# Kernel optimization log

Hardware: AMD Instinct MI355X
Metric: run time of the kernel (lower is better)

## Reference

```python
import jax, jax.numpy as jnp
import numpy as np
from jax import lax

B, N, F_IN, T = 1024, 22, 32, 32
K = 3
CHEV = 64     # nb_chev_filter
TIMEF = 64    # nb_time_filter
LN_EPS = 1e-5


def setup_inputs() -> dict:
    key = jax.random.key(0)
    ks = jax.random.split(key, 19)
    rn = lambda k, shape, s=0.1: (jax.random.normal(k, shape, jnp.float32) * s)
    return {
        "x": rn(ks[0], (B, N, F_IN, T), 1.0),
        # Temporal_Attention_layer params
        "U1": rn(ks[1], (N,)),
        "U2": rn(ks[2], (F_IN, N)),
        "U3": rn(ks[3], (F_IN,)),
        "be": rn(ks[4], (1, T, T)),
        "Ve": rn(ks[5], (T, T)),
        # Spatial_Attention_layer params
        "W1": rn(ks[6], (T,)),
        "W2": rn(ks[7], (F_IN, T)),
        "W3": rn(ks[8], (F_IN,)),
        "bs": rn(ks[9], (1, N, N)),
        "Vs": rn(ks[10], (N, N)),
        # cheb_conv_withSAt params
        "Theta": rn(ks[11], (K, F_IN, CHEV)),
        "node_emb": rn(ks[12], (N, N), 1.0),
        # time conv (1x3, pad (0,1)) and residual conv (1x1)
        "tconv_w": rn(ks[13], (TIMEF, CHEV, 1, 3)),
        "tconv_b": rn(ks[14], (TIMEF,)),
        "rconv_w": rn(ks[15], (TIMEF, F_IN, 1, 1)),
        "rconv_b": rn(ks[16], (TIMEF,)),
        # LayerNorm over nb_time_filter
        "ln_g": jnp.ones((TIMEF,), jnp.float32),
        "ln_b": jnp.zeros((TIMEF,), jnp.float32),
    }


def reference(x, U1, U2, U3, be, Ve, W1, W2, W3, bs, Vs, Theta, node_emb,
              tconv_w, tconv_b, rconv_w, rconv_b, ln_g, ln_b):
    Bx, Nx, Fx, Tx = x.shape

    # ---- Temporal attention: E_normalized [B, T, T] ----
    # lhs = ((x.permute(0,3,2,1) @ U1) @ U2)  -> [B, T, N]
    lhs_t = jnp.einsum('bnft,n->btf', x, U1) @ U2          # [B,T,N]
    rhs_t = jnp.einsum('f,bnft->bnt', U3, x)               # [B,N,T]
    prod_t = jnp.einsum('btn,bns->bts', lhs_t, rhs_t)      # [B,T,T]
    E = jnp.einsum('ts,bsu->btu', Ve, jax.nn.sigmoid(prod_t + be))
    E_norm = jax.nn.softmax(E, axis=1)                     # softmax over dim=1

    # x_TAt = reshape(x, [B, N*F, T]) @ E_norm  -> [B, N, F, T]
    x_TAt = (x.reshape(Bx, Nx * Fx, Tx) @ E_norm).reshape(Bx, Nx, Fx, Tx)

    # ---- Spatial attention on x_TAt: S_normalized [B, N, N] ----
    lhs_s = jnp.einsum('bnft,t->bnf', x_TAt, W1) @ W2      # [B,N,T]
    rhs_s = jnp.einsum('f,bnft->bnt', W3, x_TAt)           # [B,N,T]
    prod_s = jnp.einsum('bnt,bmt->bnm', lhs_s, rhs_s)      # [B,N,N]
    S = jnp.einsum('nm,bml->bnl', Vs, jax.nn.sigmoid(prod_s + bs))
    S_norm = jax.nn.softmax(S, axis=1)                     # softmax over dim=1

    # ---- Chebyshev graph conv with adaptive supports (vectorized over T) ----
    supports = jax.nn.softmax(jax.nn.relu(node_emb @ node_emb.T), axis=1)
    support_set = [jnp.eye(Nx, dtype=x.dtype), supports]
    for _ in range(2, K):
        support_set.append(2.0 * supports @ support_set[-1] - support_set[-2])

    out = jnp.zeros((Bx, Nx, CHEV, Tx), x.dtype)
    for k in range(K):
        A_k = support_set[k][None, :, :] * S_norm          # [B,N,N]
        # rhs[b,m,f,t] = sum_n A_k[b,n,m] * x[b,n,f,t]  (A_k^T @ graph_signal)
        rhs = jnp.einsum('bnm,bnft->bmft', A_k, x)
        out = out + jnp.einsum('bmft,fo->bmot', rhs, Theta[k])
    spatial_gcn = jax.nn.relu(out)                         # [B,N,CHEV,T]

    # ---- Temporal conv (1x3, pad (0,1)) on [B, CHEV, N, T] ----
    dn = ('NCHW', 'OIHW', 'NCHW')
    t_in = spatial_gcn.transpose(0, 2, 1, 3)               # [B,CHEV,N,T]
    t_out = lax.conv_general_dilated(t_in, tconv_w, (1, 1), ((0, 0), (1, 1)),
                                     dimension_numbers=dn)
    t_out = t_out + tconv_b[None, :, None, None]           # [B,TIMEF,N,T]

    # ---- Residual conv (1x1) on [B, F_in, N, T] ----
    r_in = x.transpose(0, 2, 1, 3)
    r_out = lax.conv_general_dilated(r_in, rconv_w, (1, 1), ((0, 0), (0, 0)),
                                     dimension_numbers=dn)
    r_out = r_out + rconv_b[None, :, None, None]           # [B,TIMEF,N,T]

    # ---- Residual add, ReLU, LayerNorm over channel dim ----
    y = jax.nn.relu(r_out + t_out).transpose(0, 3, 2, 1)   # [B,T,N,TIMEF]
    mu = jnp.mean(y, axis=-1, keepdims=True)
    var = jnp.var(y, axis=-1, keepdims=True)
    y = (y - mu) * lax.rsqrt(var + LN_EPS) * ln_g + ln_b
    return y.transpose(0, 2, 3, 1)                         # [B,N,TIMEF,T]
```

## Files before the change

### kernel.cpp

```cpp
#include <hip/hip_runtime.h>
#include <hip/hip_bf16.h>
#include <math.h>


typedef unsigned short u16;
typedef __attribute__((ext_vector_type(8))) short short8;
typedef __attribute__((ext_vector_type(16))) float f32x16;
typedef __attribute__((ext_vector_type(2))) float f32x2;

__device__ __forceinline__ float sigm(float v){ return 1.f/(1.f+expf(-v)); }

__device__ __forceinline__ u16 f2bf(float x){
  __hip_bfloat16 h = __float2bfloat16(x);
  return *reinterpret_cast<u16*>(&h);
}
__device__ __forceinline__ unsigned f2bf2(float lo, float hi){
  return (unsigned)f2bf(lo) | ((unsigned)f2bf(hi) << 16);
}

__global__ void k_sup_prep(const float* __restrict__ emb, float* __restrict__ wsT,
                           const float* __restrict__ Theta,
                           const float* __restrict__ tw, const float* __restrict__ tb,
                           const float* __restrict__ rw, const float* __restrict__ rb,
                           u16* __restrict__ thA, u16* __restrict__ wA, float* __restrict__ wsB){
  if (blockIdx.x < 81){
    int tid = blockIdx.x*256 + threadIdx.x;
    if (tid < 6144){
      int j = tid&7, l = (tid>>3)&63, slot = tid>>9;
      int fb = slot>>1, ch = slot&1;
      int hi = l>>5, r = l&31;
      int row = (fb < 4) ? (32 + 16*fb + 8*hi + j) : (16*(fb-4) + 8*hi + j);
      thA[tid] = f2bf(Theta[row*64 + 32*ch + r]);
    } else if (tid < 20480){
      int e = tid - 6144;
      int j = e&7, l = (e>>3)&63, slot = e>>9;
      int kb = slot>>1, oh = slot&1;
      int hi = l>>5, r = l&31;
      int k = 16*kb + 8*hi + j;
      int o = 32*oh + r;
      float v = (k < 192) ? tw[o*192 + (k&63)*3 + (k>>6)] : rw[o*32 + (k-192)];
      wA[e] = f2bf(v);
    } else if (tid < 20544){
      int o = tid - 20480; wsB[o] = tb[o] + rb[o];
    }
    return;
  }
  __shared__ float M[484];
  __shared__ float T1s[484];
  int tid = threadIdx.x;
  for (int idx=tid; idx<484; idx+=256){
    int n = idx/22, m = idx - (idx/22)*22;
    float s = 0.f;
    for (int j=0;j<22;j++) s += emb[n*22+j]*emb[m*22+j];
    M[idx] = fmaxf(s, 0.f);
  }
  __syncthreads();
  if (tid < 22){
    float mx = -1e30f;
    for (int m=0;m<22;m++) mx = fmaxf(mx, M[tid*22+m]);
    float s = 0.f;
    for (int m=0;m<22;m++) s += expf(M[tid*22+m]-mx);
    float inv = 1.f/s;
    for (int m=0;m<22;m++) T1s[tid*22+m] = expf(M[tid*22+m]-mx)*inv;
  }
  __syncthreads();
  for (int idx=tid; idx<484; idx+=256){
    int n = idx/22, m = idx - (idx/22)*22;
    float s = 0.f;
    for (int p=0;p<22;p++) s += T1s[n*22+p]*T1s[p*22+m];
    wsT[idx]      = T1s[idx];
    wsT[484+idx]  = 2.f*s - ((n==m)?1.f:0.f);
  }
}

__global__ __launch_bounds__(512) void k_attn(
    const float* __restrict__ x,
    const float* __restrict__ U1, const float* __restrict__ U2, const float* __restrict__ U3,
    const float* __restrict__ be, const float* __restrict__ Ve,
    const float* __restrict__ W1, const float* __restrict__ W2, const float* __restrict__ W3,
    const float* __restrict__ bs, const float* __restrict__ Vs,
    float* __restrict__ snorm){
  int b = blockIdx.x, tid = threadIdx.x;
  const float* xb = x + (size_t)b*22528;
  __shared__ float xu1[1024];
  __shared__ float rhs_t[704];
  __shared__ float lhs_t[704];
  __shared__ float sigp[1024];
  __shared__ float Em[1024];
  __shared__ float sm[1024];
  __shared__ float w1e[32];
  __shared__ float xw3[704];
  __shared__ float lhsS[704];
  __shared__ float lhs2[704];
  __shared__ float rhsS[704];
  __shared__ float sig2[484];
  __shared__ float Sl[484];

  for (int idx=tid; idx<1024; idx+=512){
    float a=0.f;
    for (int n=0;n<22;n++) a = fmaf(xb[n*1024 + idx], U1[n], a);
    xu1[idx]=a;
  }
  for (int idx=tid; idx<704; idx+=512){
    int n = idx>>5, t = idx&31; float a=0.f, c=0.f;
    for (int f=0;f<32;f++){ float xv = xb[n*1024+f*32+t]; a = fmaf(U3[f],xv,a); c = fmaf(W3[f],xv,c); }
    rhs_t[idx]=a; xw3[idx]=c;
  }
  __syncthreads();
  for (int idx=tid; idx<704; idx+=512){
    int t = idx/22, n2 = idx - t*22; float a=0.f;
    for (int f=0;f<32;f++) a = fmaf(xu1[f*32+t], U2[f*22+n2], a);
    lhs_t[idx]=a;
  }
  __syncthreads();
  for (int idx=tid; idx<1024; idx+=512){
    int s = idx>>5, u = idx&31; float p=0.f;
    for (int n=0;n<22;n++) p = fmaf(lhs_t[s*22+n], rhs_t[n*32+u], p);
    sigp[idx] = sigm(p + be[idx]);
  }
  __syncthreads();
  for (int idx=tid; idx<1024; idx+=512){
    int t = idx>>5, u = idx&31; float a=0.f;
    for (int s2=0;s2<32;s2++) a = fmaf(Ve[t*32+s2], sigp[s2*32+u], a);
    Em[idx]=a;
  }
  __syncthreads();
  {
    int u = tid>>4, th = tid&15;
    float e0 = Em[(2*th)*32 + u], e1 = Em[(2*th+1)*32 + u];
    float mx = fmaxf(e0, e1);
    #pragma unroll
    for (int mask=1; mask<16; mask<<=1) mx = fmaxf(mx, __shfl_xor(mx, mask));
    float x0 = expf(e0-mx), x1 = expf(e1-mx);
    float s = x0 + x1;
    #pragma unroll
    for (int mask=1; mask<16; mask<<=1) s += __shfl_xor(s, mask);
    float inv = 1.f/s;
    sm[(2*th)*32 + u]   = x0*inv;
    sm[(2*th+1)*32 + u] = x1*inv;
  }
  __syncthreads();
  {
    int u = tid>>4, th = tid&15;
    float pw = fmaf(sm[u*32 + 2*th], W1[2*th], sm[u*32 + 2*th+1]*W1[2*th+1]);
    #pragma unroll
    for (int mask=1; mask<16; mask<<=1) pw += __shfl_xor(pw, mask);
    if (th==0) w1e[u] = pw;
  }
  __syncthreads();
  for (int idx=tid; idx<704; idx+=512){
    int n = idx>>5, f = idx&31; float a=0.f;
    for (int u=0;u<32;u++) a = fmaf(xb[n*1024+f*32+u], w1e[u], a);
    lhsS[idx]=a;
  }
  __syncthreads();
  for (int idx=tid; idx<704; idx+=512){
    int n = idx>>5, t = idx&31; float a=0.f;
    for (int f=0;f<32;f++) a = fmaf(lhsS[n*32+f], W2[f*32+t], a);
    lhs2[idx]=a;
  }
  for (int idx=tid; idx<704; idx+=512){
    int mm = idx>>5, t = idx&31; float a=0.f;
    for (int u=0;u<32;u++) a = fmaf(xw3[mm*32+u], sm[u*32+t], a);
    rhsS[idx]=a;
  }
  __syncthreads();
  for (int idx=tid; idx<484; idx+=512){
    int a_ = idx/22, l = idx - (idx/22)*22; float p=0.f;
    for (int t=0;t<32;t++) p = fmaf(lhs2[a_*32+t], rhsS[l*32+t], p);
    sig2[idx] = sigm(p + bs[idx]);
  }
  __syncthreads();
  for (int idx=tid; idx<484; idx+=512){
    int n = idx/22, l = idx - (idx/22)*22; float s=0.f;
    for (int mm=0;mm<22;mm++) s = fmaf(Vs[n*22+mm], sig2[mm*22+l], s);
    Sl[idx]=s;
  }
  __syncthreads();
  {
    int grp = tid>>5, nn = tid&31;
    for (int l = grp; l < 22; l += 16){
      float v = (nn<22) ? Sl[nn*22 + l] : -1e30f;
      float mx = v;
      #pragma unroll
      for (int mask=1; mask<32; mask<<=1) mx = fmaxf(mx, __shfl_xor(mx, mask));
      float e = (nn<22) ? expf(v-mx) : 0.f;
      float s = e;
      #pragma unroll
      for (int mask=1; mask<32; mask<<=1) s += __shfl_xor(s, mask);
      if (nn<22) snorm[(size_t)b*484 + nn*22 + l] = e*(1.f/s);
    }
  }
}

__global__ __launch_bounds__(256, 5) void k_fused(
    const float* __restrict__ x,
    const float* __restrict__ wsT, const float* __restrict__ snorm,
    const u16* __restrict__ thA, const u16* __restrict__ wA, const float* __restrict__ wsB,
    const float* __restrict__ lng, const float* __restrict__ lnb,
    float* __restrict__ out){
  __shared__ __align__(16) u16 GtU[2][32*72];
  __shared__ __align__(16) u16 sgTU[2][34*72];
  __shared__ __align__(16) u16 xTU[2][32*40];
  __shared__ __align__(16) float ak4[22*4];
  __shared__ float smm[2];

  int wg = blockIdx.x;
  int logical = (wg & 7)*1408 + (wg >> 3);
  int b = logical/11, mp = logical - b*11;
  int m0 = mp*2;
  int tid = threadIdx.x;
  const float* xb = x + (size_t)b*22528;

  if (tid < 128){
    int mi = tid>>6, c = tid&63;
    sgTU[mi][c] = 0;
    sgTU[mi][33*72 + c] = 0;
  }
  if (tid < 88){
    int n = tid>>2, j = tid&3;
    int mi = j>>1, k1 = j&1;
    int m = m0 + mi;
    ak4[tid] = wsT[k1*484 + n*22 + m] * snorm[(size_t)b*484 + n*22 + m];
  }
  if (tid < 2) smm[tid] = snorm[(size_t)b*484 + (m0+tid)*23];
  __syncthreads();

  int t32 = tid&31;

  {
    int fq = tid>>5, f0 = fq*4;
    const float* xt = xb + f0*32 + t32;
    f32x2 acc[4][2];
    #pragma unroll
    for (int j=0;j<4;j++){ acc[j][0]=f32x2{0,0}; acc[j][1]=f32x2{0,0}; }
    #pragma unroll 2
    for (int n=0;n<22;n++){
      float4 av = *(const float4*)&ak4[n*4];
      const float* p = xt + n*1024;
      float x0 = p[0], x1 = p[32], x2 = p[64], x3 = p[96];
      f32x2 lo = {x0,x1}, hi2 = {x2,x3};
      f32x2 c0 = {av.x,av.x}, c1 = {av.y,av.y}, c2 = {av.z,av.z}, c3 = {av.w,av.w};
      acc[0][0] = __builtin_elementwise_fma(c0, lo,  acc[0][0]);
      acc[0][1] = __builtin_elementwise_fma(c0, hi2, acc[0][1]);
      acc[1][0] = __builtin_elementwise_fma(c1, lo,  acc[1][0]);
      acc[1][1] = __builtin_elementwise_fma(c1, hi2, acc[1][1]);
      acc[2][0] = __builtin_elementwise_fma(c2, lo,  acc[2][0]);
      acc[2][1] = __builtin_elementwise_fma(c2, hi2, acc[2][1]);
      acc[3][0] = __builtin_elementwise_fma(c3, lo,  acc[3][0]);
      acc[3][1] = __builtin_elementwise_fma(c3, hi2, acc[3][1]);
    }
    #pragma unroll
    for (int mi=0;mi<2;mi++){
      #pragma unroll
      for (int k1=0;k1<2;k1++){
        int j = mi*2 + k1;
        uint2 v; v.x = f2bf2(acc[j][0][0], acc[j][0][1]); v.y = f2bf2(acc[j][1][0], acc[j][1][1]);
        *(uint2*)&GtU[mi][t32*72 + k1*32 + f0] = v;
      }
      const float* q = xb + (m0+mi)*1024 + f0*32 + t32;
      float y0 = q[0], y1 = q[32], y2 = q[64], y3 = q[96];
      uint2 v; v.x = f2bf2(y0,y1); v.y = f2bf2(y2,y3);
      *(uint2*)&xTU[mi][t32*40 + f0] = v;
    }
  }
  __syncthreads();

  int w = tid>>6, l = tid&63, hi = l>>5;
  int mi = w>>1, ch = w&1;
  int lt = l&31;

  {
    f32x16 aG, aX;
    #pragma unroll
    for (int i=0;i<16;i++){ aG[i]=0.f; aX[i]=0.f; }
    const u16* gRow = &GtU[mi][lt*72 + 8*hi];
    const u16* xRow = &xTU[mi][lt*40 + 8*hi];
    #pragma unroll
    for (int fb=0; fb<4; ++fb){
      short8 a = *(const short8*)(thA + (size_t)(fb*2+ch)*512 + l*8);
      aG = __builtin_amdgcn_mfma_f32_32x32x16_bf16(a, *(const short8*)(gRow + 16*fb), aG, 0,0,0);
    }
    #pragma unroll
    for (int fb=4; fb<6; ++fb){
      short8 a = *(const short8*)(thA + (size_t)(fb*2+ch)*512 + l*8);
      aX = __builtin_amdgcn_mfma_f32_32x32x16_bf16(a, *(const short8*)(xRow + 16*(fb-4)), aX, 0,0,0);
    }
    float smv = smm[mi];
    u16* srow = &sgTU[mi][(1+lt)*72 + ch*32 + 4*hi];
    #pragma unroll
    for (int q=0;q<4;q++){
      float v0 = fmaxf(fmaf(smv, aX[4*q+0], aG[4*q+0]), 0.f);
      float v1 = fmaxf(fmaf(smv, aX[4*q+1], aG[4*q+1]), 0.f);
      float v2 = fmaxf(fmaf(smv, aX[4*q+2], aG[4*q+2]), 0.f);
      float v3 = fmaxf(fmaf(smv, aX[4*q+3], aG[4*q+3]), 0.f);
      uint2 pv; pv.x = f2bf2(v0,v1); pv.y = f2bf2(v2,v3);
      *(uint2*)&srow[8*q] = pv;
    }
  }
  __syncthreads();

  f32x16 acc;
  #pragma unroll
  for (int i=0;i<16;i++) acc[i]=0.f;
  {
    #pragma unroll
    for (int kb=0; kb<12; ++kb){
      int dt = kb>>2, cq = kb&3;
      short8 wk = *(const short8*)(wA + (size_t)(kb*2+ch)*512 + l*8);
      const short8* Bp = (const short8*)&sgTU[mi][(lt+dt)*72 + cq*16 + 8*hi];
      acc = __builtin_amdgcn_mfma_f32_32x32x16_bf16(wk, *Bp, acc, 0,0,0);
    }
    #pragma unroll
    for (int kb=12; kb<14; ++kb){
      short8 wk = *(const short8*)(wA + (size_t)(kb*2+ch)*512 + l*8);
      const short8* Bp = (const short8*)&xTU[mi][lt*40 + (kb-12)*16 + 8*hi];
      acc = __builtin_amdgcn_mfma_f32_32x32x16_bf16(wk, *Bp, acc, 0,0,0);
    }
  }

  float y[16];
  float s1 = 0.f, s2 = 0.f;
  {
    const float4* wsB4 = (const float4*)wsB;
    #pragma unroll
    for (int q=0;q<4;q++){
      float4 bq = wsB4[8*ch + 2*q + hi];
      float bb[4] = {bq.x, bq.y, bq.z, bq.w};
      #pragma unroll
      for (int e=0;e<4;e++){
        float v = fmaxf(acc[4*q+e] + bb[e], 0.f);
        y[4*q+e] = v;
        s1 += v;
        s2 = fmaf(v, v, s2);
      }
    }
  }
  s1 += __shfl_xor(s1, 32);
  s2 += __shfl_xor(s2, 32);
  float* p1 = (float*)&GtU[0][0];
  float* p2 = p1 + 128;
  if (l < 32){
    p1[(mi*32 + lt)*2 + ch] = s1;
    p2[(mi*32 + lt)*2 + ch] = s2;
  }
  __syncthreads();
  f32x2 q1 = *(const f32x2*)&p1[(mi*32 + lt)*2];
  f32x2 q2 = *(const f32x2*)&p2[(mi*32 + lt)*2];
  float S1 = q1[0] + q1[1], S2 = q2[0] + q2[1];
  float mu = S1*(1.f/64.f);
  float var = S2*(1.f/64.f) - mu*mu;
  float rs = rsqrtf(var + 1e-5f);
  {
    const float4* lng4 = (const float4*)lng;
    const float4* lnb4 = (const float4*)lnb;
    float* ob = out + ((size_t)(b*22 + m0 + mi)*64 + 32*ch)*32;
    #pragma unroll
    for (int q=0;q<4;q++){
      float4 g4 = lng4[8*ch + 2*q + hi];
      float4 b4 = lnb4[8*ch + 2*q + hi];
      float gg[4] = {g4.x,g4.y,g4.z,g4.w};
      float bg[4] = {b4.x,b4.y,b4.z,b4.w};
      #pragma unroll
      for (int e=0;e<4;e++){
        int orow = 8*q + 4*hi + e;
        ob[orow*32 + lt] = (y[4*q+e]-mu)*rs*gg[e] + bg[e];
      }
    }
  }
}

extern "C" void kernel_launch(void* const* d_in, const int* in_sizes, int n_in,
                              void* d_out, int out_size, void* d_ws, size_t ws_size,
                              hipStream_t stream){
  const float* x     = (const float*)d_in[0];
  const float* U1    = (const float*)d_in[1];
  const float* U2    = (const float*)d_in[2];
  const float* U3    = (const float*)d_in[3];
  const float* be    = (const float*)d_in[4];
  const float* Ve    = (const float*)d_in[5];
  const float* W1    = (const float*)d_in[6];
  const float* W2    = (const float*)d_in[7];
  const float* W3    = (const float*)d_in[8];
  const float* bs    = (const float*)d_in[9];
  const float* Vs    = (const float*)d_in[10];
  const float* Theta = (const float*)d_in[11];
  const float* emb   = (const float*)d_in[12];
  const float* tw    = (const float*)d_in[13];
  const float* tb    = (const float*)d_in[14];
  const float* rw    = (const float*)d_in[15];
  const float* rb    = (const float*)d_in[16];
  const float* lng   = (const float*)d_in[17];
  const float* lnb   = (const float*)d_in[18];
  float* out = (float*)d_out;
  float* wsf = (float*)d_ws;
  float* wsT   = wsf;
  float* snorm = wsf + 1024;
  u16*   thA   = (u16*)(wsf + 496640);
  u16*   wA    = (u16*)(wsf + 499712);
  float* wsB   = wsf + 506880;

  k_sup_prep<<<82, 256, 0, stream>>>(emb, wsT, Theta, tw, tb, rw, rb, thA, wA, wsB);
  k_attn<<<1024, 512, 0, stream>>>(x, U1,U2,U3, be,Ve, W1,W2,W3, bs,Vs, snorm);
  k_fused<<<1024*11, 256, 0, stream>>>(x, wsT, snorm, thA, wA, wsB, lng, lnb, out);
}
```

Before: 160.8 us.

## Vectorize x loads, XOR-swizzle LDS tiles, and prefetch MFMA weight fragments

The x gather now uses one float4 load per thread per node instead of four strided scalar loads. The scattered bf16 writes into the G and xT LDS tiles use an XOR-swizzled column layout to avoid bank conflicts, and the MFMA B-operand reads apply the matching swizzle. Theta and conv weight fragments are loaded into registers early, before barriers, to hide global latency. Launch bounds drop from 5 to 3 blocks per SM to make room for the extra registers, which risks lower occupancy, and the LDS writes become scalar 16-bit stores.

```diff
diff --git a/kernel.cpp b/kernel.cpp
--- a/kernel.cpp
+++ b/kernel.cpp
@@ -193,7 +193,7 @@
   }
 }
 
-__global__ __launch_bounds__(256, 5) void k_fused(
+__global__ __launch_bounds__(256, 3) void k_fused(
     const float* __restrict__ x,
     const float* __restrict__ wsT, const float* __restrict__ snorm,
     const u16* __restrict__ thA, const u16* __restrict__ wA, const float* __restrict__ wsB,
@@ -212,6 +212,14 @@
   int tid = threadIdx.x;
   const float* xb = x + (size_t)b*22528;
 
+  int w = tid>>6, l = tid&63, hi = l>>5, lt = l&31;
+  int mi_w = w>>1, ch = w&1;
+
+  short8 a_th[6];
+  #pragma unroll
+  for (int fb=0; fb<6; ++fb)
+    a_th[fb] = *(const short8*)(thA + (size_t)(fb*2+ch)*512 + l*8);
+
   if (tid < 128){
     int mi = tid>>6, c = tid&63;
     sgTU[mi][c] = 0;
@@ -226,68 +234,74 @@
   if (tid < 2) smm[tid] = snorm[(size_t)b*484 + (m0+tid)*23];
   __syncthreads();
 
-  int t32 = tid&31;
-
-  {
-    int fq = tid>>5, f0 = fq*4;
-    const float* xt = xb + f0*32 + t32;
+  {
     f32x2 acc[4][2];
     #pragma unroll
     for (int j=0;j<4;j++){ acc[j][0]=f32x2{0,0}; acc[j][1]=f32x2{0,0}; }
+    const float4* x4 = (const float4*)xb;
     #pragma unroll 2
     for (int n=0;n<22;n++){
       float4 av = *(const float4*)&ak4[n*4];
-      const float* p = xt + n*1024;
-      float x0 = p[0], x1 = p[32], x2 = p[64], x3 = p[96];
-      f32x2 lo = {x0,x1}, hi2 = {x2,x3};
+      float4 xv = x4[n*256 + tid];
+      f32x2 xlo = {xv.x, xv.y}, xhi2 = {xv.z, xv.w};
       f32x2 c0 = {av.x,av.x}, c1 = {av.y,av.y}, c2 = {av.z,av.z}, c3 = {av.w,av.w};
-      acc[0][0] = __builtin_elementwise_fma(c0, lo,  acc[0][0]);
-      acc[0][1] = __builtin_elementwise_fma(c0, hi2, acc[0][1]);
-      acc[1][0] = __builtin_elementwise_fma(c1, lo,  acc[1][0]);
-      acc[1][1] = __builtin_elementwise_fma(c1, hi2, acc[1][1]);
-      acc[2][0] = __builtin_elementwise_fma(c2, lo,  acc[2][0]);
-      acc[2][1] = __builtin_elementwise_fma(c2, hi2, acc[2][1]);
-      acc[3][0] = __builtin_elementwise_fma(c3, lo,  acc[3][0]);
-      acc[3][1] = __builtin_elementwise_fma(c3, hi2, acc[3][1]);
-    }
+      acc[0][0] = __builtin_elementwise_fma(c0, xlo,  acc[0][0]);
+      acc[0][1] = __builtin_elementwise_fma(c0, xhi2, acc[0][1]);
+      acc[1][0] = __builtin_elementwise_fma(c1, xlo,  acc[1][0]);
+      acc[1][1] = __builtin_elementwise_fma(c1, xhi2, acc[1][1]);
+      acc[2][0] = __builtin_elementwise_fma(c2, xlo,  acc[2][0]);
+      acc[2][1] = __builtin_elementwise_fma(c2, xhi2, acc[2][1]);
+      acc[3][0] = __builtin_elementwise_fma(c3, xlo,  acc[3][0]);
+      acc[3][1] = __builtin_elementwise_fma(c3, xhi2, acc[3][1]);
+    }
+    int f = tid>>3, t7 = tid&7, t0 = t7*4;
+    int w4 = f>>3, f_low = f&7;
+    int gcol0 = 8*((0*4 + w4) ^ t7) + f_low;
+    int gcol1 = 8*((1*4 + w4) ^ t7) + f_low;
+    int xcol  = 8*(w4 ^ (t7&3)) + f_low;
     #pragma unroll
     for (int mi=0;mi<2;mi++){
+      float4 xm = ((const float4*)xb)[(m0+mi)*256 + tid];
+      u16* xd = &xTU[mi][0];
+      xd[(t0+0)*40 + xcol] = f2bf(xm.x);
+      xd[(t0+1)*40 + xcol] = f2bf(xm.y);
+      xd[(t0+2)*40 + xcol] = f2bf(xm.z);
+      xd[(t0+3)*40 + xcol] = f2bf(xm.w);
       #pragma unroll
       for (int k1=0;k1<2;k1++){
         int j = mi*2 + k1;
-        uint2 v; v.x = f2bf2(acc[j][0][0], acc[j][0][1]); v.y = f2bf2(acc[j][1][0], acc[j][1][1]);
-        *(uint2*)&GtU[mi][t32*72 + k1*32 + f0] = v;
+        int gc = k1 ? gcol1 : gcol0;
+        u16* gd = &GtU[mi][gc];
+        gd[(t0+0)*72] = f2bf(acc[j][0][0]);
+        gd[(t0+1)*72] = f2bf(acc[j][0][1]);
+        gd[(t0+2)*72] = f2bf(acc[j][1][0]);
+        gd[(t0+3)*72] = f2bf(acc[j][1][1]);
       }
-      const float* q = xb + (m0+mi)*1024 + f0*32 + t32;
-      float y0 = q[0], y1 = q[32], y2 = q[64], y3 = q[96];
-      uint2 v; v.x = f2bf2(y0,y1); v.y = f2bf2(y2,y3);
-      *(uint2*)&xTU[mi][t32*40 + f0] = v;
-    }
-  }
-  __syncthreads();
-
-  int w = tid>>6, l = tid&63, hi = l>>5;
-  int mi = w>>1, ch = w&1;
-  int lt = l&31;
+    }
+  }
+  __syncthreads();
+
+  int key8 = lt>>2;
+  int key4 = key8 & 3;
 
   {
     f32x16 aG, aX;
     #pragma unroll
     for (int i=0;i<16;i++){ aG[i]=0.f; aX[i]=0.f; }
-    const u16* gRow = &GtU[mi][lt*72 + 8*hi];
-    const u16* xRow = &xTU[mi][lt*40 + 8*hi];
+    const u16* gBase = &GtU[mi_w][lt*72];
+    const u16* xBase = &xTU[mi_w][lt*40];
     #pragma unroll
     for (int fb=0; fb<4; ++fb){
-      short8 a = *(const short8*)(thA + (size_t)(fb*2+ch)*512 + l*8);
-      aG = __builtin_amdgcn_mfma_f32_32x32x16_bf16(a, *(const short8*)(gRow + 16*fb), aG, 0,0,0);
+      const short8* gp = (const short8*)(gBase + 8*((2*fb+hi)^key8));
+      aG = __builtin_amdgcn_mfma_f32_32x32x16_bf16(a_th[fb], *gp, aG, 0,0,0);
     }
     #pragma unroll
     for (int fb=4; fb<6; ++fb){
-      short8 a = *(const short8*)(thA + (size_t)(fb*2+ch)*512 + l*8);
-      aX = __builtin_amdgcn_mfma_f32_32x32x16_bf16(a, *(const short8*)(xRow + 16*(fb-4)), aX, 0,0,0);
-    }
-    float smv = smm[mi];
-    u16* srow = &sgTU[mi][(1+lt)*72 + ch*32 + 4*hi];
+      const short8* xp = (const short8*)(xBase + 8*((2*(fb-4)+hi)^key4));
+      aX = __builtin_amdgcn_mfma_f32_32x32x16_bf16(a_th[fb], *xp, aX, 0,0,0);
+    }
+    float smv = smm[mi_w];
+    u16* srow = &sgTU[mi_w][(1+lt)*72 + ch*32 + 4*hi];
     #pragma unroll
     for (int q=0;q<4;q++){
       float v0 = fmaxf(fmaf(smv, aX[4*q+0], aG[4*q+0]), 0.f);
@@ -298,6 +312,11 @@
       *(uint2*)&srow[8*q] = pv;
     }
   }
+
+  short8 wk[14];
+  #pragma unroll
+  for (int kb=0; kb<14; ++kb)
+    wk[kb] = *(const short8*)(wA + (size_t)(kb*2+ch)*512 + l*8);
   __syncthreads();
 
   f32x16 acc;
@@ -307,15 +326,13 @@
     #pragma unroll
     for (int kb=0; kb<12; ++kb){
       int dt = kb>>2, cq = kb&3;
-      short8 wk = *(const short8*)(wA + (size_t)(kb*2+ch)*512 + l*8);
-      const short8* Bp = (const short8*)&sgTU[mi][(lt+dt)*72 + cq*16 + 8*hi];
-      acc = __builtin_amdgcn_mfma_f32_32x32x16_bf16(wk, *Bp, acc, 0,0,0);
+      const short8* Bp = (const short8*)&sgTU[mi_w][(lt+dt)*72 + cq*16 + 8*hi];
+      acc = __builtin_amdgcn_mfma_f32_32x32x16_bf16(wk[kb], *Bp, acc, 0,0,0);
     }
     #pragma unroll
     for (int kb=12; kb<14; ++kb){
-      short8 wk = *(const short8*)(wA + (size_t)(kb*2+ch)*512 + l*8);
-      const short8* Bp = (const short8*)&xTU[mi][lt*40 + (kb-12)*16 + 8*hi];
-      acc = __builtin_amdgcn_mfma_f32_32x32x16_bf16(wk, *Bp, acc, 0,0,0);
+      const short8* Bp = (const short8*)&xTU[mi_w][lt*40 + 8*((2*(kb-12)+hi)^key4)];
+      acc = __builtin_amdgcn_mfma_f32_32x32x16_bf16(wk[kb], *Bp, acc, 0,0,0);
     }
   }
 
@@ -341,12 +358,12 @@
   float* p1 = (float*)&GtU[0][0];
   float* p2 = p1 + 128;
   if (l < 32){
-    p1[(mi*32 + lt)*2 + ch] = s1;
-    p2[(mi*32 + lt)*2 + ch] = s2;
-  }
-  __syncthreads();
-  f32x2 q1 = *(const f32x2*)&p1[(mi*32 + lt)*2];
-  f32x2 q2 = *(const f32x2*)&p2[(mi*32 + lt)*2];
+    p1[(mi_w*32 + lt)*2 + ch] = s1;
+    p2[(mi_w*32 + lt)*2 + ch] = s2;
+  }
+  __syncthreads();
+  f32x2 q1 = *(const f32x2*)&p1[(mi_w*32 + lt)*2];
+  f32x2 q2 = *(const f32x2*)&p2[(mi_w*32 + lt)*2];
   float S1 = q1[0] + q1[1], S2 = q2[0] + q2[1];
   float mu = S1*(1.f/64.f);
   float var = S2*(1.f/64.f) - mu*mu;
@@ -354,7 +371,7 @@
   {
     const float4* lng4 = (const float4*)lng;
     const float4* lnb4 = (const float4*)lnb;
-    float* ob = out + ((size_t)(b*22 + m0 + mi)*64 + 32*ch)*32;
+    float* ob = out + ((size_t)(b*22 + m0 + mi_w)*64 + 32*ch)*32;
     #pragma unroll
     for (int q=0;q<4;q++){
       float4 g4 = lng4[8*ch + 2*q + hi];
```

New measurement: 157.7 us. Within noise of the previous version (-1.9%).
